# Performance work log

Hardware: AMD Instinct MI355X
Metric: run time of the kernel (lower is better)

The kernel has to match this reference:

```python
import jax, jax.numpy as jnp
import numpy as np

EMB_DIM = 1024
NUM_HEADS = 16
SCALE_WEIGHTS = 1.0
TINY = jnp.finfo(jnp.float32).tiny


def setup_inputs() -> dict:
    key = jax.random.key(0)
    k1, k2, k3 = jax.random.split(key, 3)
    B, S = 2, 2048
    x = jax.random.normal(k1, (B, S, EMB_DIM), dtype=jnp.float32)
    weights = jax.random.uniform(k2, (B, S), dtype=jnp.float32)
    W_qkv = jax.random.normal(k3, (EMB_DIM, 3 * EMB_DIM), dtype=jnp.float32) / np.sqrt(EMB_DIM)
    b_qkv = jnp.zeros((3 * EMB_DIM,), dtype=jnp.float32)
    return {"x": x, "weights": weights, "W_qkv": W_qkv, "b_qkv": b_qkv}


def reference(x, weights, W_qkv, b_qkv):
    B, S, E = x.shape
    H = NUM_HEADS
    hd = E // H
    # QKV projection: [B,S,3E] -> [B,H,S,3*hd] -> split
    qkv = x @ W_qkv + b_qkv
    qkv = qkv.reshape(B, S, H, 3 * hd).transpose(0, 2, 1, 3)
    q, k, v = jnp.split(qkv, 3, axis=-1)  # each [B,H,S,hd]
    # weights: [B,S] -> [B,1,1,S] (broadcast over heads and query positions)
    w = weights[:, None, None, :]
    # scores with log-weight bias and hard masks
    attn_logits = jnp.einsum("bhqd,bhkd->bhqk", q, k) / jnp.sqrt(jnp.asarray(hd, x.dtype))
    attn_logits = attn_logits + jnp.log(w / SCALE_WEIGHTS + TINY)
    attn_logits = jnp.where(w == 0, -9e15, attn_logits)
    attn_logits = jnp.where(w == 1, 9e15, attn_logits)
    attention = jax.nn.softmax(attn_logits, axis=-1)
    values = jnp.einsum("bhqk,bhkd->bhqd", attention, v)
    return values.transpose(0, 2, 1, 3).reshape(B, S, E)
```

## Files before the change

kernel.cpp:

```cpp
#include <hip/hip_runtime.h>
#include <math.h>

#define B_  2
#define S_  2048
#define E_  1024
#define H_  16
#define HD_ 64
#define N3_ 3072
#define M_  (B_*S_)

typedef _Float16 h8  __attribute__((ext_vector_type(8)));
typedef _Float16 h4  __attribute__((ext_vector_type(4)));
typedef float    f4  __attribute__((ext_vector_type(4)));
typedef float    fv16 __attribute__((ext_vector_type(16)));

typedef __attribute__((address_space(3))) unsigned int       lds_u32;
typedef const __attribute__((address_space(1))) unsigned int glob_u32;

__device__ __forceinline__ void gld16(const void* g, void* l) {
    __builtin_amdgcn_global_load_lds((glob_u32*)g, (lds_u32*)l, 16, 0, 0);
}
__device__ __forceinline__ float exp2_hw(float x) { return __builtin_amdgcn_exp2f(x); }

#define QSCALE 0.18033688011112042f

__global__ void wcvt_kernel(const float* __restrict__ w, _Float16* __restrict__ w16) {
    int i = blockIdx.x * 256 + threadIdx.x;
    if (i < B_ * S_) w16[i] = (_Float16)w[i];
}

__global__ void cvt_x_kernel(const float* __restrict__ x, _Float16* __restrict__ x16) {
    int i = (blockIdx.x * 256 + threadIdx.x) * 8;
    float4 u = *(const float4*)&x[i];
    float4 v = *(const float4*)&x[i + 4];
    h8 o;
    o[0] = (_Float16)u.x; o[1] = (_Float16)u.y; o[2] = (_Float16)u.z; o[3] = (_Float16)u.w;
    o[4] = (_Float16)v.x; o[5] = (_Float16)v.y; o[6] = (_Float16)v.z; o[7] = (_Float16)v.w;
    *(h8*)&x16[i] = o;
}

__global__ __launch_bounds__(256) void transpose_w_kernel(
        const float* __restrict__ W, _Float16* __restrict__ Wt) {
    __shared__ float T[64][65];
    int k0 = blockIdx.x * 64, n0 = blockIdx.y * 64;
    int tid = threadIdx.x;
    int r = tid >> 4, c4 = (tid & 15) * 4;
#pragma unroll
    for (int i = 0; i < 4; i++) {
        int row = r + i * 16;
        float4 u = *(const float4*)&W[(size_t)(k0 + row) * N3_ + n0 + c4];
        T[c4 + 0][row] = u.x; T[c4 + 1][row] = u.y;
        T[c4 + 2][row] = u.z; T[c4 + 3][row] = u.w;
    }
    __syncthreads();
#pragma unroll
    for (int i = 0; i < 4; i++) {
        int rn = r + i * 16;
        h4 p;
        p[0] = (_Float16)T[rn][c4 + 0]; p[1] = (_Float16)T[rn][c4 + 1];
        p[2] = (_Float16)T[rn][c4 + 2]; p[3] = (_Float16)T[rn][c4 + 3];
        *(h4*)&Wt[(size_t)(n0 + rn) * E_ + k0 + c4] = p;
    }
}

__global__ __launch_bounds__(256, 2) void qkv_gemm32(
        const _Float16* __restrict__ x16, const _Float16* __restrict__ wt,
        const float* __restrict__ bq, const float* __restrict__ w,
        _Float16* __restrict__ qws, _Float16* __restrict__ kws,
        _Float16* __restrict__ vtws) {
    __shared__ __align__(16) _Float16 As[128 * 64];
    __shared__ __align__(16) _Float16 Ws[192 * 64];

    int tid = threadIdx.x;
    int wid = tid >> 6, lane = tid & 63;
    int l31 = lane & 31, hi = lane >> 5;
    int wm = wid & 1, wn = wid >> 1;

    int L = blockIdx.x;
    int head = 2 * (L & 7) + (L >> 8);
    int mb = (L >> 3) & 31;
    int m0 = mb * 128;
    int n0 = head * 192;
    int b = m0 >> 11;
    int bh = b * H_ + head;
    int sblk = m0 & 2047;

    int srow = lane >> 3;
    int schunk = (lane & 7) ^ srow;
    int l7 = l31 & 7;

    fv16 acc[2][3];
#pragma unroll
    for (int ntl = 0; ntl < 3; ntl++) {
        int n_abs = wn * 96 + ntl * 32;
        int which = n_abs >> 6;
        fv16 ini;
        if (which == 2) {
            float bb = bq[n0 + n_abs + l31];
#pragma unroll
            for (int r = 0; r < 16; r++) ini[r] = bb;
        } else {
#pragma unroll
            for (int g = 0; g < 4; g++) {
                f4 bv = *(const f4*)&bq[n0 + n_abs + 8 * g + 4 * hi];
#pragma unroll
                for (int j = 0; j < 4; j++) ini[4 * g + j] = bv[j];
            }
        }
        acc[0][ntl] = ini; acc[1][ntl] = ini;
    }

    const _Float16* agp = &x16[(size_t)(m0 + wid * 32 + srow) * E_ + schunk * 8];
    const _Float16* wgp = &wt[(size_t)(n0 + wid * 48 + srow) * E_ + schunk * 8];

    for (int k0 = 0; k0 < E_; k0 += 64) {
#pragma unroll
        for (int j = 0; j < 4; j++)
            gld16(agp + (size_t)j * 8 * E_ + k0, &As[(wid * 32 + j * 8) * 64]);
#pragma unroll
        for (int j = 0; j < 6; j++)
            gld16(wgp + (size_t)j * 8 * E_ + k0, &Ws[(wid * 48 + j * 8) * 64]);
        __syncthreads();
#pragma unroll
        for (int step = 0; step < 4; step++) {
            int ph = ((2 * step + hi) ^ l7) * 8;
            h8 af[2], wf[3];
#pragma unroll
            for (int mt = 0; mt < 2; mt++)
                af[mt] = *(const h8*)&As[(wm * 64 + mt * 32 + l31) * 64 + ph];
#pragma unroll
            for (int ntl = 0; ntl < 3; ntl++)
                wf[ntl] = *(const h8*)&Ws[(wn * 96 + ntl * 32 + l31) * 64 + ph];
#pragma unroll
            for (int ntl = 0; ntl < 3; ntl++) {
                bool isv = (wn == 1) && (ntl >= 1);
#pragma unroll
                for (int mt = 0; mt < 2; mt++) {
                    if (isv)
                        acc[mt][ntl] = __builtin_amdgcn_mfma_f32_32x32x16_f16(af[mt], wf[ntl], acc[mt][ntl], 0, 0, 0);
                    else
                        acc[mt][ntl] = __builtin_amdgcn_mfma_f32_32x32x16_f16(wf[ntl], af[mt], acc[mt][ntl], 0, 0, 0);
                }
            }
        }
        __syncthreads();
    }

#pragma unroll
    for (int ntl = 0; ntl < 3; ntl++) {
        int n_abs = wn * 96 + ntl * 32;
        int which = n_abs >> 6;
#pragma unroll
        for (int mt = 0; mt < 2; mt++) {
            if (which == 2) {
                int d = (n_abs & 63) + l31;
#pragma unroll
                for (int g = 0; g < 4; g++) {
                    int soff = wm * 64 + mt * 32 + 8 * g + 4 * hi;
                    f4 wf4 = *(const f4*)&w[m0 + soff];
                    h4 p;
#pragma unroll
                    for (int j = 0; j < 4; j++)
                        p[j] = (_Float16)(acc[mt][ntl][4 * g + j] * wf4[j]);
                    *(h4*)&vtws[((size_t)bh * 64 + d) * S_ + sblk + soff] = p;
                }
            } else {
                _Float16* dst = (which == 0) ? qws : kws;
                float scale = (which == 0) ? QSCALE : 1.0f;
                int s = sblk + wm * 64 + mt * 32 + l31;
#pragma unroll
                for (int g = 0; g < 4; g++) {
                    int d0 = (n_abs & 63) + 8 * g + 4 * hi;
                    h4 p;
#pragma unroll
                    for (int j = 0; j < 4; j++)
                        p[j] = (_Float16)(acc[mt][ntl][4 * g + j] * scale);
                    *(h4*)&dst[((size_t)bh * S_ + s) * 64 + d0] = p;
                }
            }
        }
    }
}

__global__ __launch_bounds__(256, 2) void attn_kernel(
        const _Float16* __restrict__ q, const _Float16* __restrict__ k,
        const _Float16* __restrict__ vt, const _Float16* __restrict__ w16,
        float* __restrict__ out) {
    __shared__ __align__(16) _Float16 Ks[64 * 64];
    __shared__ __align__(16) _Float16 Vts[64 * 64];

    int tid = threadIdx.x;
    int wid = tid >> 6, lane = tid & 63;
    int l31 = lane & 31, hi = lane >> 5;
    int l7 = l31 & 7;
    int L = blockIdx.x;
    int bh = (L & 7) + 8 * (L >> 7);
    int qt = (L >> 3) & 15;
    int q0 = qt * 128;
    int b = bh >> 4, h = bh & 15;

    const _Float16* qbase = q + (size_t)bh * S_ * HD_;
    const _Float16* kbase = k + (size_t)bh * S_ * HD_;
    const _Float16* vbase = vt + (size_t)bh * HD_ * S_;
    const _Float16* wbase = w16 + (size_t)b * S_;

    int srow = lane >> 3;
    int schunk = (lane & 7) ^ srow;

    int qrow = q0 + wid * 32 + l31;
    h8 qf[4];
#pragma unroll
    for (int step = 0; step < 4; step++)
        qf[step] = *(const h8*)&qbase[(size_t)qrow * 64 + 16 * step + 8 * hi];

    fv16 o[2];
    o[0] = (fv16)0.0f; o[1] = (fv16)0.0f;
    float m_r = -INFINITY, l_r = 0.0f;

    const _Float16* kgp = &kbase[(size_t)(wid * 16 + srow) * 64 + schunk * 8];
    const _Float16* vgp = &vbase[(size_t)(wid * 16 + srow) * S_ + schunk * 8];

    for (int kt = 0; kt < 32; kt++) {
        int k0 = kt * 64;
#pragma unroll
        for (int j = 0; j < 2; j++) {
            gld16(kgp + (size_t)(k0 + j * 8) * 64, &Ks[(wid * 16 + j * 8) * 64]);
            gld16(vgp + (size_t)j * 8 * S_ + k0, &Vts[(wid * 16 + j * 8) * 64]);
        }
        h4 wv[2][4];
#pragma unroll
        for (int kt2 = 0; kt2 < 2; kt2++)
#pragma unroll
            for (int g = 0; g < 4; g++)
                wv[kt2][g] = *(const h4*)&wbase[k0 + kt2 * 32 + 8 * g + 4 * hi];
        __syncthreads();

        fv16 st[2];
        st[0] = (fv16)0.0f; st[1] = (fv16)0.0f;
#pragma unroll
        for (int step = 0; step < 4; step++) {
            int ph = ((2 * step + hi) ^ l7) * 8;
#pragma unroll
            for (int kt2 = 0; kt2 < 2; kt2++) {
                h8 kf = *(const h8*)&Ks[(kt2 * 32 + l31) * 64 + ph];
                st[kt2] = __builtin_amdgcn_mfma_f32_32x32x16_f16(kf, qf[step], st[kt2], 0, 0, 0);
            }
        }

        float rm = -INFINITY;
#pragma unroll
        for (int kt2 = 0; kt2 < 2; kt2++)
#pragma unroll
            for (int r = 0; r < 16; r++) rm = fmaxf(rm, st[kt2][r]);
        rm = fmaxf(rm, __shfl_xor(rm, 32));
        float mnew = fmaxf(m_r, rm);
        float rs = 0.0f;
        h4 pf[2][4];
#pragma unroll
        for (int kt2 = 0; kt2 < 2; kt2++)
#pragma unroll
            for (int g = 0; g < 4; g++) {
                f4 e;
#pragma unroll
                for (int j = 0; j < 4; j++) {
                    float ev = exp2_hw(st[kt2][4 * g + j] - mnew);
                    e[j] = ev;
                    rs += ev * (float)wv[kt2][g][j];
                }
                h4 p;
                p[0] = (_Float16)e[0]; p[1] = (_Float16)e[1];
                p[2] = (_Float16)e[2]; p[3] = (_Float16)e[3];
                pf[kt2][g] = p;
            }
        rs += __shfl_xor(rs, 32);
        float alpha = exp2_hw(m_r - mnew);
        m_r = mnew;
        l_r = l_r * alpha + rs;
        o[0] = o[0] * alpha;
        o[1] = o[1] * alpha;

#pragma unroll
        for (int kt2 = 0; kt2 < 2; kt2++)
#pragma unroll
            for (int g = 0; g < 4; g++) {
                int ph = ((4 * kt2 + g) ^ l7) * 8 + hi * 4;
#pragma unroll
                for (int dt = 0; dt < 2; dt++) {
                    h4 vf = *(const h4*)&Vts[(dt * 32 + l31) * 64 + ph];
                    o[dt] = __builtin_amdgcn_mfma_f32_32x32x8f16(vf, pf[kt2][g], o[dt], 0, 0, 0);
                }
            }
        __syncthreads();
    }

    float linv = 1.0f / l_r;
    float* obase = &out[((size_t)(b * S_ + qrow)) * E_ + h * 64];
#pragma unroll
    for (int dt = 0; dt < 2; dt++)
#pragma unroll
        for (int g = 0; g < 4; g++) {
            int d0 = dt * 32 + 8 * g + 4 * hi;
            f4 ov;
#pragma unroll
            for (int j = 0; j < 4; j++) ov[j] = o[dt][4 * g + j] * linv;
            *(f4*)&obase[d0] = ov;
        }
}

extern "C" void kernel_launch(void* const* d_in, const int* in_sizes, int n_in,
                              void* d_out, int out_size, void* d_ws, size_t ws_size,
                              hipStream_t stream) {
    const float* x  = (const float*)d_in[0];
    const float* w  = (const float*)d_in[1];
    const float* Wq = (const float*)d_in[2];
    const float* bq = (const float*)d_in[3];
    float* out = (float*)d_out;

    char* p = (char*)d_ws;
    _Float16* x16 = (_Float16*)p;              p += (size_t)M_ * E_ * 2;
    _Float16* wt  = (_Float16*)p;              p += (size_t)E_ * N3_ * 2;
    _Float16* qb  = (_Float16*)p;              p += (size_t)M_ * E_ * 2;
    _Float16* kb  = (_Float16*)p;              p += (size_t)M_ * E_ * 2;
    _Float16* vtb = (_Float16*)p;              p += (size_t)M_ * E_ * 2;
    _Float16* w16 = (_Float16*)p;

    wcvt_kernel<<<dim3(16), dim3(256), 0, stream>>>(w, w16);
    cvt_x_kernel<<<dim3(M_ * E_ / 2048), dim3(256), 0, stream>>>(x, x16);
    transpose_w_kernel<<<dim3(E_ / 64, N3_ / 64), dim3(256), 0, stream>>>(Wq, wt);
    qkv_gemm32<<<dim3(512), dim3(256), 0, stream>>>(x16, wt, bq, w, qb, kb, vtb);
    attn_kernel<<<dim3(512), dim3(256), 0, stream>>>(qb, kb, vtb, w16, out);
}
```

Measured before the change: 186.4 us.

## Double-buffer LDS tiles in QKV GEMM and attention, stage weights in LDS

Result: faster. 179.5 us (-3.7%).

```diff
diff --git a/kernel.cpp b/kernel.cpp
--- a/kernel.cpp
+++ b/kernel.cpp
@@ -23,11 +23,6 @@
 __device__ __forceinline__ float exp2_hw(float x) { return __builtin_amdgcn_exp2f(x); }
 
 #define QSCALE 0.18033688011112042f
-
-__global__ void wcvt_kernel(const float* __restrict__ w, _Float16* __restrict__ w16) {
-    int i = blockIdx.x * 256 + threadIdx.x;
-    if (i < B_ * S_) w16[i] = (_Float16)w[i];
-}
 
 __global__ void cvt_x_kernel(const float* __restrict__ x, _Float16* __restrict__ x16) {
     int i = (blockIdx.x * 256 + threadIdx.x) * 8;
@@ -68,12 +63,13 @@
         const float* __restrict__ bq, const float* __restrict__ w,
         _Float16* __restrict__ qws, _Float16* __restrict__ kws,
         _Float16* __restrict__ vtws) {
-    __shared__ __align__(16) _Float16 As[128 * 64];
-    __shared__ __align__(16) _Float16 Ws[192 * 64];
+    __shared__ __align__(16) _Float16 Ab[2][128 * 64];
+    __shared__ __align__(16) _Float16 Wb[2][192 * 64];
 
     int tid = threadIdx.x;
     int wid = tid >> 6, lane = tid & 63;
-    int l31 = lane & 31, hi = lane >> 5;
+    int l31 = lane & 31, hi = lane >> 5, l7 = l31 & 7;
+    int srow = lane >> 3;
     int wm = wid & 1, wn = wid >> 1;
 
     int L = blockIdx.x;
@@ -85,10 +81,6 @@
     int bh = b * H_ + head;
     int sblk = m0 & 2047;
 
-    int srow = lane >> 3;
-    int schunk = (lane & 7) ^ srow;
-    int l7 = l31 & 7;
-
     fv16 acc[2][3];
 #pragma unroll
     for (int ntl = 0; ntl < 3; ntl++) {
@@ -110,27 +102,45 @@
         acc[0][ntl] = ini; acc[1][ntl] = ini;
     }
 
-    const _Float16* agp = &x16[(size_t)(m0 + wid * 32 + srow) * E_ + schunk * 8];
-    const _Float16* wgp = &wt[(size_t)(n0 + wid * 48 + srow) * E_ + schunk * 8];
-
-    for (int k0 = 0; k0 < E_; k0 += 64) {
-#pragma unroll
-        for (int j = 0; j < 4; j++)
-            gld16(agp + (size_t)j * 8 * E_ + k0, &As[(wid * 32 + j * 8) * 64]);
-#pragma unroll
-        for (int j = 0; j < 6; j++)
-            gld16(wgp + (size_t)j * 8 * E_ + k0, &Ws[(wid * 48 + j * 8) * 64]);
+    auto stage = [&](int t, int bf) {
+        int k0 = t * 64;
+#pragma unroll
+        for (int j = 0; j < 4; j++) {
+            int batch = wid * 4 + j;
+            int row = batch * 8 + srow;
+            int ch = (lane & 7) ^ srow ^ (batch & 7);
+            gld16(&x16[(size_t)(m0 + row) * E_ + k0 + ch * 8], &Ab[bf][batch * 8 * 64]);
+        }
+#pragma unroll
+        for (int j = 0; j < 6; j++) {
+            int batch = wid * 6 + j;
+            int row = batch * 8 + srow;
+            int ch = (lane & 7) ^ srow ^ (batch & 7);
+            gld16(&wt[(size_t)(n0 + row) * E_ + k0 + ch * 8], &Wb[bf][batch * 8 * 64]);
+        }
+    };
+
+    stage(0, 0);
+
+    for (int t = 0; t < 16; t++) {
+        int bf = t & 1;
         __syncthreads();
+        if (t < 15) stage(t + 1, bf ^ 1);
 #pragma unroll
         for (int step = 0; step < 4; step++) {
-            int ph = ((2 * step + hi) ^ l7) * 8;
             h8 af[2], wf[3];
 #pragma unroll
-            for (int mt = 0; mt < 2; mt++)
-                af[mt] = *(const h8*)&As[(wm * 64 + mt * 32 + l31) * 64 + ph];
-#pragma unroll
-            for (int ntl = 0; ntl < 3; ntl++)
-                wf[ntl] = *(const h8*)&Ws[(wn * 96 + ntl * 32 + l31) * 64 + ph];
+            for (int mt = 0; mt < 2; mt++) {
+                int R = wm * 64 + mt * 32 + l31;
+                int ph = ((2 * step + hi) ^ l7 ^ ((mt * 4 + (l31 >> 3)) & 7)) * 8;
+                af[mt] = *(const h8*)&Ab[bf][R * 64 + ph];
+            }
+#pragma unroll
+            for (int ntl = 0; ntl < 3; ntl++) {
+                int R = wn * 96 + ntl * 32 + l31;
+                int ph = ((2 * step + hi) ^ l7 ^ ((wn * 12 + ntl * 4 + (l31 >> 3)) & 7)) * 8;
+                wf[ntl] = *(const h8*)&Wb[bf][R * 64 + ph];
+            }
 #pragma unroll
             for (int ntl = 0; ntl < 3; ntl++) {
                 bool isv = (wn == 1) && (ntl >= 1);
@@ -143,7 +153,6 @@
                 }
             }
         }
-        __syncthreads();
     }
 
 #pragma unroll
@@ -184,15 +193,16 @@
 
 __global__ __launch_bounds__(256, 2) void attn_kernel(
         const _Float16* __restrict__ q, const _Float16* __restrict__ k,
-        const _Float16* __restrict__ vt, const _Float16* __restrict__ w16,
+        const _Float16* __restrict__ vt, const float* __restrict__ w,
         float* __restrict__ out) {
-    __shared__ __align__(16) _Float16 Ks[64 * 64];
-    __shared__ __align__(16) _Float16 Vts[64 * 64];
+    __shared__ __align__(16) _Float16 Kb[2][64 * 64];
+    __shared__ __align__(16) _Float16 Vb[2][64 * 64];
+    __shared__ __align__(16) float lws[2048];
 
     int tid = threadIdx.x;
     int wid = tid >> 6, lane = tid & 63;
-    int l31 = lane & 31, hi = lane >> 5;
-    int l7 = l31 & 7;
+    int l31 = lane & 31, hi = lane >> 5, l7 = l31 & 7;
+    int srow = lane >> 3;
     int L = blockIdx.x;
     int bh = (L & 7) + 8 * (L >> 7);
     int qt = (L >> 3) & 15;
@@ -202,10 +212,27 @@
     const _Float16* qbase = q + (size_t)bh * S_ * HD_;
     const _Float16* kbase = k + (size_t)bh * S_ * HD_;
     const _Float16* vbase = vt + (size_t)bh * HD_ * S_;
-    const _Float16* wbase = w16 + (size_t)b * S_;
-
-    int srow = lane >> 3;
-    int schunk = (lane & 7) ^ srow;
+    const float* wbase = w + (size_t)b * S_;
+
+#pragma unroll
+    for (int j = 0; j < 2; j++) {
+        int batch = wid + 4 * j;
+        gld16(&wbase[batch * 256 + lane * 4], &lws[batch * 256]);
+    }
+
+    auto stage = [&](int kt, int bf) {
+        int k0 = kt * 64;
+#pragma unroll
+        for (int j = 0; j < 2; j++) {
+            int batch = wid * 2 + j;
+            int row = batch * 8 + srow;
+            int ch = (lane & 7) ^ srow ^ (batch & 7);
+            gld16(&kbase[(size_t)(k0 + row) * 64 + ch * 8], &Kb[bf][batch * 8 * 64]);
+            gld16(&vbase[(size_t)row * S_ + k0 + ch * 8], &Vb[bf][batch * 8 * 64]);
+        }
+    };
+
+    stage(0, 0);
 
     int qrow = q0 + wid * 32 + l31;
     h8 qf[4];
@@ -217,32 +244,20 @@
     o[0] = (fv16)0.0f; o[1] = (fv16)0.0f;
     float m_r = -INFINITY, l_r = 0.0f;
 
-    const _Float16* kgp = &kbase[(size_t)(wid * 16 + srow) * 64 + schunk * 8];
-    const _Float16* vgp = &vbase[(size_t)(wid * 16 + srow) * S_ + schunk * 8];
-
     for (int kt = 0; kt < 32; kt++) {
-        int k0 = kt * 64;
-#pragma unroll
-        for (int j = 0; j < 2; j++) {
-            gld16(kgp + (size_t)(k0 + j * 8) * 64, &Ks[(wid * 16 + j * 8) * 64]);
-            gld16(vgp + (size_t)j * 8 * S_ + k0, &Vts[(wid * 16 + j * 8) * 64]);
-        }
-        h4 wv[2][4];
-#pragma unroll
-        for (int kt2 = 0; kt2 < 2; kt2++)
-#pragma unroll
-            for (int g = 0; g < 4; g++)
-                wv[kt2][g] = *(const h4*)&wbase[k0 + kt2 * 32 + 8 * g + 4 * hi];
+        int bf = kt & 1;
         __syncthreads();
+        if (kt < 31) stage(kt + 1, bf ^ 1);
 
         fv16 st[2];
         st[0] = (fv16)0.0f; st[1] = (fv16)0.0f;
 #pragma unroll
         for (int step = 0; step < 4; step++) {
-            int ph = ((2 * step + hi) ^ l7) * 8;
 #pragma unroll
             for (int kt2 = 0; kt2 < 2; kt2++) {
-                h8 kf = *(const h8*)&Ks[(kt2 * 32 + l31) * 64 + ph];
+                int R = kt2 * 32 + l31;
+                int ph = ((2 * step + hi) ^ l7 ^ ((kt2 * 4 + (l31 >> 3)) & 7)) * 8;
+                h8 kf = *(const h8*)&Kb[bf][R * 64 + ph];
                 st[kt2] = __builtin_amdgcn_mfma_f32_32x32x16_f16(kf, qf[step], st[kt2], 0, 0, 0);
             }
         }
@@ -256,16 +271,18 @@
         float mnew = fmaxf(m_r, rm);
         float rs = 0.0f;
         h4 pf[2][4];
+        int k0 = kt * 64;
 #pragma unroll
         for (int kt2 = 0; kt2 < 2; kt2++)
 #pragma unroll
             for (int g = 0; g < 4; g++) {
+                f4 wv = *(const f4*)&lws[k0 + kt2 * 32 + 8 * g + 4 * hi];
                 f4 e;
 #pragma unroll
                 for (int j = 0; j < 4; j++) {
                     float ev = exp2_hw(st[kt2][4 * g + j] - mnew);
                     e[j] = ev;
-                    rs += ev * (float)wv[kt2][g][j];
+                    rs += ev * wv[j];
                 }
                 h4 p;
                 p[0] = (_Float16)e[0]; p[1] = (_Float16)e[1];
@@ -283,14 +300,15 @@
         for (int kt2 = 0; kt2 < 2; kt2++)
 #pragma unroll
             for (int g = 0; g < 4; g++) {
-                int ph = ((4 * kt2 + g) ^ l7) * 8 + hi * 4;
+                int c = 4 * kt2 + g;
 #pragma unroll
                 for (int dt = 0; dt < 2; dt++) {
-                    h4 vf = *(const h4*)&Vts[(dt * 32 + l31) * 64 + ph];
+                    int R = dt * 32 + l31;
+                    int ph = (c ^ l7 ^ ((dt * 4 + (l31 >> 3)) & 7)) * 8 + hi * 4;
+                    h4 vf = *(const h4*)&Vb[bf][R * 64 + ph];
                     o[dt] = __builtin_amdgcn_mfma_f32_32x32x8f16(vf, pf[kt2][g], o[dt], 0, 0, 0);
                 }
             }
-        __syncthreads();
     }
 
     float linv = 1.0f / l_r;
@@ -321,12 +339,10 @@
     _Float16* wt  = (_Float16*)p;              p += (size_t)E_ * N3_ * 2;
     _Float16* qb  = (_Float16*)p;              p += (size_t)M_ * E_ * 2;
     _Float16* kb  = (_Float16*)p;              p += (size_t)M_ * E_ * 2;
-    _Float16* vtb = (_Float16*)p;              p += (size_t)M_ * E_ * 2;
-    _Float16* w16 = (_Float16*)p;
-
-    wcvt_kernel<<<dim3(16), dim3(256), 0, stream>>>(w, w16);
+    _Float16* vtb = (_Float16*)p;
+
     cvt_x_kernel<<<dim3(M_ * E_ / 2048), dim3(256), 0, stream>>>(x, x16);
     transpose_w_kernel<<<dim3(E_ / 64, N3_ / 64), dim3(256), 0, stream>>>(Wq, wt);
     qkv_gemm32<<<dim3(512), dim3(256), 0, stream>>>(x16, wt, bq, w, qb, kb, vtb);
-    attn_kernel<<<dim3(512), dim3(256), 0, stream>>>(qb, kb, vtb, w16, out);
-}
+    attn_kernel<<<dim3(512), dim3(256), 0, stream>>>(qb, kb, vtb, w, out);
+}
```
